# Kernel tuning notes

Measured on AMD Instinct MI355X. Metric: run time of the kernel, lower is better.

Reference implementation:

```python
import jax, jax.numpy as jnp
import numpy as np

M, K, N = 8192, 4096, 4096

def setup_inputs() -> dict:
    key = jax.random.key(0)
    k1, k2 = jax.random.split(key)
    x_q = jax.random.randint(k1, (M, K), -128, 128, dtype=jnp.int8)
    weight_q = jax.random.randint(k2, (N, K), -128, 128, dtype=jnp.int8)
    scale_x = jnp.float32(0.02)
    weight_scale = jnp.float32(1.0)
    out_scale = jnp.float32(1.0)
    return {"x_q": x_q, "scale_x": scale_x, "weight_q": weight_q,
            "weight_scale": weight_scale, "out_scale": out_scale}

def reference(x_q, scale_x, weight_q, weight_scale, out_scale):
    # int8 GEMM with int32 accumulation: [M,K] @ [K,N] -> [M,N] int32
    acc = jnp.matmul(x_q.astype(jnp.int32), weight_q.T.astype(jnp.int32))
    # fused dequant + requant scale, then round/clamp back to int8
    scale = scale_x * weight_scale / out_scale
    y = acc.astype(jnp.float32) * scale
    y_q = jnp.clip(jnp.round(y), -128, 127).astype(jnp.int8)
    return (y_q, out_scale)
```

## Files before the change

kernel.cpp:

```cpp
#include <hip/hip_runtime.h>
#include <stdint.h>

#define M_DIM 8192
#define K_DIM 4096
#define N_DIM 4096

typedef __attribute__((ext_vector_type(4))) int i32x4;

__global__ __launch_bounds__(256) void pack_kernel(const int* __restrict__ src,
                                                   int8_t* __restrict__ dst,
                                                   int n4) {
  const int stride = gridDim.x * 256;
  for (int i = blockIdx.x * 256 + threadIdx.x; i < n4; i += stride) {
    int4 v = reinterpret_cast<const int4*>(src)[i];
    int p = (v.x & 0xff) | ((v.y & 0xff) << 8) |
            ((v.z & 0xff) << 16) | ((v.w & 0xff) << 24);
    reinterpret_cast<int*>(dst)[i] = p;
  }
}

__global__ void tail_kernel(float* __restrict__ out, const float* __restrict__ so) {
  out[(size_t)M_DIM * N_DIM] = so[0];
}

#define BM2 256
#define BN2 256
#define BK2 128
#define NT  (K_DIM / BK2)

#define ASM_VMCNT0 asm volatile("s_waitcnt vmcnt(0)" ::: "memory")
#define ASM_LGKM0  asm volatile("s_waitcnt lgkmcnt(0)" ::: "memory")
#define BARRIER()  asm volatile("s_barrier" ::: "memory")
#define SCHEDB()   __builtin_amdgcn_sched_barrier(0)

#define STAGE(KT, BUF) do { \
  _Pragma("unroll") \
  for (int c_ = 0; c_ < 4; ++c_) { \
    const int8_t* ga_ = A8 + (size_t)(arow0 + c_*64 + srow) * K_DIM + (size_t)(KT)*BK2 + scol; \
    __builtin_amdgcn_global_load_lds((const __attribute__((address_space(1))) void*)ga_, \
        (__attribute__((address_space(3))) void*)(lds + (BUF)*65536 + c_*8192 + tid*16), 16, 0, 0); \
  } \
  _Pragma("unroll") \
  for (int c_ = 0; c_ < 4; ++c_) { \
    const int8_t* gb_ = B8 + (size_t)(bcol0 + c_*64 + srow) * K_DIM + (size_t)(KT)*BK2 + scol; \
    __builtin_amdgcn_global_load_lds((const __attribute__((address_space(1))) void*)gb_, \
        (__attribute__((address_space(3))) void*)(lds + (BUF)*65536 + 32768 + c_*8192 + tid*16), 16, 0, 0); \
  } } while (0)

__global__ __launch_bounds__(512, 2) void gemm2p(
    const int8_t* __restrict__ A8, const int8_t* __restrict__ B8,
    float* __restrict__ out,
    const float* __restrict__ sx, const float* __restrict__ sw,
    const float* __restrict__ so) {
  __shared__ __align__(16) int8_t lds[131072];

  const int tid = threadIdx.x;
  const int lane = tid & 63;
  const int wid = tid >> 6;
  const int wr = wid >> 2;
  const int wc = wid & 3;
  const int lrow = lane & 15;
  const int kq = lane >> 4;

  const int bid = blockIdx.x;
  const int wg = (bid & 7) * 64 + (bid >> 3);
  const int bm = wg & 31;
  const int bn = wg >> 5;
  const size_t arow0 = (size_t)bm * BM2;
  const size_t bcol0 = (size_t)bn * BN2;

  const int srow = tid >> 3;
  const int scol = (((tid & 7) ^ ((tid >> 3) & 7)) << 4);

  const int swz = (lrow & 7) << 4;
  const int pc0 = (0  + kq * 16) ^ swz;
  const int pc1 = (64 + kq * 16) ^ swz;
  const int aoff = (wr * 128 + lrow) * 128;
  const int boff = 32768 + (wc * 64 + lrow) * 128;

  i32x4 acc[8][4] = {};
  i32x4 af[8], bf[4];

  STAGE(0, 0);
  ASM_VMCNT0; BARRIER(); SCHEDB();

  for (int kt = 0; kt < NT; ++kt) {
    const int cb = kt & 1;
    const int8_t* abase = lds + cb * 65536 + aoff;
    const int8_t* bbase = lds + cb * 65536 + boff;
    if (kt < NT - 1) STAGE(kt + 1, cb ^ 1);

#pragma unroll
    for (int m = 0; m < 8; ++m) af[m] = *(const i32x4*)(abase + m * 2048 + pc0);
#pragma unroll
    for (int n = 0; n < 4; ++n) bf[n] = *(const i32x4*)(bbase + n * 2048 + pc0);
    ASM_LGKM0; SCHEDB();
    __builtin_amdgcn_s_setprio(1);
#pragma unroll
    for (int m = 0; m < 8; ++m)
#pragma unroll
      for (int n = 0; n < 4; ++n)
        acc[m][n] = __builtin_amdgcn_mfma_i32_16x16x64_i8(af[m], bf[n], acc[m][n], 0, 0, 0);
    __builtin_amdgcn_s_setprio(0);

#pragma unroll
    for (int m = 0; m < 8; ++m) af[m] = *(const i32x4*)(abase + m * 2048 + pc1);
#pragma unroll
    for (int n = 0; n < 4; ++n) bf[n] = *(const i32x4*)(bbase + n * 2048 + pc1);
    ASM_LGKM0; SCHEDB();
    __builtin_amdgcn_s_setprio(1);
#pragma unroll
    for (int m = 0; m < 8; ++m)
#pragma unroll
      for (int n = 0; n < 4; ++n)
        acc[m][n] = __builtin_amdgcn_mfma_i32_16x16x64_i8(af[m], bf[n], acc[m][n], 0, 0, 0);
    __builtin_amdgcn_s_setprio(0);

    ASM_VMCNT0; BARRIER(); SCHEDB();
  }

  const float s0 = *(volatile const float*)sx;
  const float s1 = *(volatile const float*)sw;
  const float s2 = *(volatile const float*)so;
  const float scale = s0 * s1 / s2;
#pragma unroll
  for (int m = 0; m < 8; ++m) {
#pragma unroll
    for (int n = 0; n < 4; ++n) {
#pragma unroll
      for (int j = 0; j < 4; ++j) {
        int gr = (int)arow0 + wr * 128 + m * 16 + kq * 4 + j;
        int gc = (int)bcol0 + wc * 64 + n * 16 + lrow;
        float v = rintf((float)acc[m][n][j] * scale);
        v = fminf(fmaxf(v, -128.f), 127.f);
        out[(size_t)gr * N_DIM + gc] = v;
      }
    }
  }
}

#define BM 128
#define BN 128
#define BK 64
__global__ __launch_bounds__(256) void gemm_direct(
    const int* __restrict__ A32, const int* __restrict__ B32,
    float* __restrict__ out,
    const float* __restrict__ sx, const float* __restrict__ sw,
    const float* __restrict__ so) {
  __shared__ int8_t As[BM * BK];
  __shared__ int8_t Bs[BN * BK];
  const int tid = threadIdx.x;
  const int lane = tid & 63;
  const int wid = tid >> 6;
  const int bid = blockIdx.x;
  const int bm = bid % (M_DIM / BM);
  const int bn = bid / (M_DIM / BM);
  const size_t arow0 = (size_t)bm * BM;
  const size_t bcol0 = (size_t)bn * BN;
  const int wrr = wid >> 1, wcc = wid & 1;
  const int lrow = lane & 15, kq = lane >> 4;
  i32x4 acc[4][4] = {};
  for (int kk = 0; kk < K_DIM; kk += BK) {
#pragma unroll
    for (int i = 0; i < 2; ++i) {
      int loff = i * 4096 + tid * 16;
      int r = loff >> 6, c = loff & 63;
      const int4* a4 = reinterpret_cast<const int4*>(A32 + (arow0 + r) * K_DIM + kk + c);
      const int4* b4 = reinterpret_cast<const int4*>(B32 + (bcol0 + r) * K_DIM + kk + c);
      int4 pa, pb;
      int4 t0 = a4[0], t1 = a4[1], t2 = a4[2], t3 = a4[3];
      pa.x = (t0.x & 0xff) | ((t0.y & 0xff) << 8) | ((t0.z & 0xff) << 16) | ((t0.w & 0xff) << 24);
      pa.y = (t1.x & 0xff) | ((t1.y & 0xff) << 8) | ((t1.z & 0xff) << 16) | ((t1.w & 0xff) << 24);
      pa.z = (t2.x & 0xff) | ((t2.y & 0xff) << 8) | ((t2.z & 0xff) << 16) | ((t2.w & 0xff) << 24);
      pa.w = (t3.x & 0xff) | ((t3.y & 0xff) << 8) | ((t3.z & 0xff) << 16) | ((t3.w & 0xff) << 24);
      t0 = b4[0]; t1 = b4[1]; t2 = b4[2]; t3 = b4[3];
      pb.x = (t0.x & 0xff) | ((t0.y & 0xff) << 8) | ((t0.z & 0xff) << 16) | ((t0.w & 0xff) << 24);
      pb.y = (t1.x & 0xff) | ((t1.y & 0xff) << 8) | ((t1.z & 0xff) << 16) | ((t1.w & 0xff) << 24);
      pb.z = (t2.x & 0xff) | ((t2.y & 0xff) << 8) | ((t2.z & 0xff) << 16) | ((t2.w & 0xff) << 24);
      pb.w = (t3.x & 0xff) | ((t3.y & 0xff) << 8) | ((t3.z & 0xff) << 16) | ((t3.w & 0xff) << 24);
      *reinterpret_cast<int4*>(As + loff) = pa;
      *reinterpret_cast<int4*>(Bs + loff) = pb;
    }
    __syncthreads();
    i32x4 afr[4], bfr[4];
#pragma unroll
    for (int m = 0; m < 4; ++m)
      afr[m] = *reinterpret_cast<const i32x4*>(As + (wrr * 64 + m * 16 + lrow) * BK + kq * 16);
#pragma unroll
    for (int n = 0; n < 4; ++n)
      bfr[n] = *reinterpret_cast<const i32x4*>(Bs + (wcc * 64 + n * 16 + lrow) * BK + kq * 16);
#pragma unroll
    for (int m = 0; m < 4; ++m)
#pragma unroll
      for (int n = 0; n < 4; ++n)
        acc[m][n] = __builtin_amdgcn_mfma_i32_16x16x64_i8(afr[m], bfr[n], acc[m][n], 0, 0, 0);
    __syncthreads();
  }
  const float scale = sx[0] * sw[0] / so[0];
#pragma unroll
  for (int m = 0; m < 4; ++m)
#pragma unroll
    for (int n = 0; n < 4; ++n)
#pragma unroll
      for (int j = 0; j < 4; ++j) {
        int gr = (int)arow0 + wrr * 64 + m * 16 + kq * 4 + j;
        int gc = (int)bcol0 + wcc * 64 + n * 16 + lrow;
        float v = rintf((float)acc[m][n][j] * scale);
        v = fminf(fmaxf(v, -128.f), 127.f);
        out[(size_t)gr * N_DIM + gc] = v;
      }
}

extern "C" void kernel_launch(void* const* d_in, const int* in_sizes, int n_in,
                              void* d_out, int out_size, void* d_ws, size_t ws_size,
                              hipStream_t stream) {
  const int* x32 = (const int*)d_in[0];
  const float* sx = (const float*)d_in[1];
  const int* w32 = (const int*)d_in[2];
  const float* sw = (const float*)d_in[3];
  const float* so = (const float*)d_in[4];
  float* out = (float*)d_out;

  tail_kernel<<<1, 1, 0, stream>>>(out, so);

  const size_t a_bytes = (size_t)M_DIM * K_DIM;
  const size_t b_bytes = (size_t)N_DIM * K_DIM;

  if (ws_size >= a_bytes + b_bytes) {
    int8_t* A8 = (int8_t*)d_ws;
    int8_t* B8 = A8 + a_bytes;
    pack_kernel<<<2048, 256, 0, stream>>>(x32, A8, (int)(a_bytes / 4));
    pack_kernel<<<2048, 256, 0, stream>>>(w32, B8, (int)(b_bytes / 4));
    const int grid = (M_DIM / BM2) * (N_DIM / BN2);
    gemm2p<<<grid, 512, 0, stream>>>(A8, B8, out, sx, sw, so);
  } else {
    const int grid = (M_DIM / BM) * (N_DIM / BN);
    gemm_direct<<<grid, 256, 0, stream>>>(x32, w32, out, sx, sw, so);
  }
}
```

Measured before the change: 401.2 us.

## Split tile loads into quadrants and interleave with sub-tile MFMA phases

Restructures the int8 GEMM main loop into four phases, each computing one quadrant of the 256x256 tile while the next k-tile's A/B halves are streamed into the other LDS buffer. Partial vmcnt waits replace the full drain, so global-to-LDS loads overlap compute at finer granularity. Each warp's fragment mapping changes to interleaved 64x32 sub-blocks, and both K halves are read together. The cost is more barriers per iteration and more registers for the doubled fragment arrays.

```diff
diff --git a/kernel.cpp b/kernel.cpp
--- a/kernel.cpp
+++ b/kernel.cpp
@@ -28,26 +28,58 @@
 #define BK2 128
 #define NT  (K_DIM / BK2)
 
-#define ASM_VMCNT0 asm volatile("s_waitcnt vmcnt(0)" ::: "memory")
-#define ASM_LGKM0  asm volatile("s_waitcnt lgkmcnt(0)" ::: "memory")
-#define BARRIER()  asm volatile("s_barrier" ::: "memory")
-#define SCHEDB()   __builtin_amdgcn_sched_barrier(0)
-
-#define STAGE(KT, BUF) do { \
-  _Pragma("unroll") \
-  for (int c_ = 0; c_ < 4; ++c_) { \
-    const int8_t* ga_ = A8 + (size_t)(arow0 + c_*64 + srow) * K_DIM + (size_t)(KT)*BK2 + scol; \
-    __builtin_amdgcn_global_load_lds((const __attribute__((address_space(1))) void*)ga_, \
-        (__attribute__((address_space(3))) void*)(lds + (BUF)*65536 + c_*8192 + tid*16), 16, 0, 0); \
-  } \
-  _Pragma("unroll") \
-  for (int c_ = 0; c_ < 4; ++c_) { \
-    const int8_t* gb_ = B8 + (size_t)(bcol0 + c_*64 + srow) * K_DIM + (size_t)(KT)*BK2 + scol; \
-    __builtin_amdgcn_global_load_lds((const __attribute__((address_space(1))) void*)gb_, \
-        (__attribute__((address_space(3))) void*)(lds + (BUF)*65536 + 32768 + c_*8192 + tid*16), 16, 0, 0); \
-  } } while (0)
-
-__global__ __launch_bounds__(512, 2) void gemm2p(
+#define ASM_VMCNT(N) asm volatile("s_waitcnt vmcnt(" #N ")" ::: "memory")
+#define ASM_LGKM0    asm volatile("s_waitcnt lgkmcnt(0)" ::: "memory")
+#define BARRIER()    asm volatile("s_barrier" ::: "memory")
+#define SCHEDB()     __builtin_amdgcn_sched_barrier(0)
+
+#define STAGE_A(KT, H, BUF) do { \
+  _Pragma("unroll") \
+  for (int c_ = 0; c_ < 2; ++c_) { \
+    const int8_t* g_ = A8 + (size_t)(arow0 + (H)*128 + c_*64 + srow) * K_DIM + (size_t)(KT)*BK2 + scol; \
+    __builtin_amdgcn_global_load_lds((const __attribute__((address_space(1))) void*)g_, \
+        (__attribute__((address_space(3))) void*)(lds + (BUF)*65536 + (H)*16384 + c_*8192 + tid*16), 16, 0, 0); \
+  } } while (0)
+
+#define STAGE_B(KT, H, BUF) do { \
+  _Pragma("unroll") \
+  for (int c_ = 0; c_ < 2; ++c_) { \
+    const int8_t* g_ = B8 + (size_t)(bcol0 + (H)*128 + c_*64 + srow) * K_DIM + (size_t)(KT)*BK2 + scol; \
+    __builtin_amdgcn_global_load_lds((const __attribute__((address_space(1))) void*)g_, \
+        (__attribute__((address_space(3))) void*)(lds + (BUF)*65536 + 32768 + (H)*16384 + c_*8192 + tid*16), 16, 0, 0); \
+  } } while (0)
+
+#define READ_AF(MH, AB) do { \
+  _Pragma("unroll") \
+  for (int m_ = 0; m_ < 4; ++m_) { \
+    const int8_t* p_ = (AB) + (MH)*16384 + m_*2048; \
+    af[(MH)*4 + m_][0] = *(const i32x4*)(p_ + pc0); \
+    af[(MH)*4 + m_][1] = *(const i32x4*)(p_ + pc1); \
+  } } while (0)
+
+#define READ_BF(NH, BB) do { \
+  _Pragma("unroll") \
+  for (int n_ = 0; n_ < 2; ++n_) { \
+    const int8_t* p_ = (BB) + (NH)*16384 + n_*2048; \
+    bf[(NH)*2 + n_][0] = *(const i32x4*)(p_ + pc0); \
+    bf[(NH)*2 + n_][1] = *(const i32x4*)(p_ + pc1); \
+  } } while (0)
+
+#define MMA16(MH, NH) do { \
+  __builtin_amdgcn_s_setprio(1); \
+  _Pragma("unroll") \
+  for (int m_ = 0; m_ < 4; ++m_) \
+    _Pragma("unroll") \
+    for (int n_ = 0; n_ < 2; ++n_) { \
+      acc[(MH)*4 + m_][(NH)*2 + n_] = __builtin_amdgcn_mfma_i32_16x16x64_i8( \
+          af[(MH)*4 + m_][0], bf[(NH)*2 + n_][0], acc[(MH)*4 + m_][(NH)*2 + n_], 0, 0, 0); \
+      acc[(MH)*4 + m_][(NH)*2 + n_] = __builtin_amdgcn_mfma_i32_16x16x64_i8( \
+          af[(MH)*4 + m_][1], bf[(NH)*2 + n_][1], acc[(MH)*4 + m_][(NH)*2 + n_], 0, 0, 0); \
+    } \
+  __builtin_amdgcn_s_setprio(0); \
+} while (0)
+
+__global__ __launch_bounds__(512, 2) void gemm8p(
     const int8_t* __restrict__ A8, const int8_t* __restrict__ B8,
     float* __restrict__ out,
     const float* __restrict__ sx, const float* __restrict__ sw,
@@ -75,48 +107,55 @@
   const int swz = (lrow & 7) << 4;
   const int pc0 = (0  + kq * 16) ^ swz;
   const int pc1 = (64 + kq * 16) ^ swz;
-  const int aoff = (wr * 128 + lrow) * 128;
-  const int boff = 32768 + (wc * 64 + lrow) * 128;
+  const int aoff = (wr * 64 + lrow) * 128;
+  const int boff = 32768 + (wc * 32 + lrow) * 128;
 
   i32x4 acc[8][4] = {};
-  i32x4 af[8], bf[4];
-
-  STAGE(0, 0);
-  ASM_VMCNT0; BARRIER(); SCHEDB();
-
-  for (int kt = 0; kt < NT; ++kt) {
+  i32x4 af[8][2], bf[4][2];
+
+  STAGE_A(0, 0, 0); STAGE_B(0, 0, 0); STAGE_B(0, 1, 0); STAGE_A(0, 1, 0);
+
+  for (int kt = 0; kt < NT - 1; ++kt) {
     const int cb = kt & 1;
-    const int8_t* abase = lds + cb * 65536 + aoff;
-    const int8_t* bbase = lds + cb * 65536 + boff;
-    if (kt < NT - 1) STAGE(kt + 1, cb ^ 1);
-
-#pragma unroll
-    for (int m = 0; m < 8; ++m) af[m] = *(const i32x4*)(abase + m * 2048 + pc0);
-#pragma unroll
-    for (int n = 0; n < 4; ++n) bf[n] = *(const i32x4*)(bbase + n * 2048 + pc0);
-    ASM_LGKM0; SCHEDB();
-    __builtin_amdgcn_s_setprio(1);
-#pragma unroll
-    for (int m = 0; m < 8; ++m)
-#pragma unroll
-      for (int n = 0; n < 4; ++n)
-        acc[m][n] = __builtin_amdgcn_mfma_i32_16x16x64_i8(af[m], bf[n], acc[m][n], 0, 0, 0);
-    __builtin_amdgcn_s_setprio(0);
-
-#pragma unroll
-    for (int m = 0; m < 8; ++m) af[m] = *(const i32x4*)(abase + m * 2048 + pc1);
-#pragma unroll
-    for (int n = 0; n < 4; ++n) bf[n] = *(const i32x4*)(bbase + n * 2048 + pc1);
-    ASM_LGKM0; SCHEDB();
-    __builtin_amdgcn_s_setprio(1);
-#pragma unroll
-    for (int m = 0; m < 8; ++m)
-#pragma unroll
-      for (int n = 0; n < 4; ++n)
-        acc[m][n] = __builtin_amdgcn_mfma_i32_16x16x64_i8(af[m], bf[n], acc[m][n], 0, 0, 0);
-    __builtin_amdgcn_s_setprio(0);
-
-    ASM_VMCNT0; BARRIER(); SCHEDB();
+    const int pb = cb ^ 1;
+    const int8_t* ab = lds + cb * 65536 + aoff;
+    const int8_t* bb = lds + cb * 65536 + boff;
+    ASM_VMCNT(4); BARRIER(); SCHEDB();
+    READ_AF(0, ab); READ_BF(0, bb);
+    STAGE_A(kt + 1, 0, pb);
+    ASM_LGKM0; SCHEDB();
+    MMA16(0, 0);
+    ASM_VMCNT(4); BARRIER(); SCHEDB();
+    READ_BF(1, bb);
+    STAGE_B(kt + 1, 0, pb);
+    ASM_LGKM0; SCHEDB();
+    MMA16(0, 1);
+    ASM_VMCNT(4); BARRIER(); SCHEDB();
+    READ_AF(1, ab);
+    STAGE_B(kt + 1, 1, pb);
+    ASM_LGKM0; SCHEDB();
+    MMA16(1, 0);
+    BARRIER(); SCHEDB();
+    STAGE_A(kt + 1, 1, pb);
+    MMA16(1, 1);
+  }
+  {
+    const int cb = (NT - 1) & 1;
+    const int8_t* ab = lds + cb * 65536 + aoff;
+    const int8_t* bb = lds + cb * 65536 + boff;
+    ASM_VMCNT(4); BARRIER(); SCHEDB();
+    READ_AF(0, ab); READ_BF(0, bb);
+    ASM_LGKM0; SCHEDB();
+    MMA16(0, 0);
+    ASM_VMCNT(2); BARRIER(); SCHEDB();
+    READ_BF(1, bb);
+    ASM_LGKM0; SCHEDB();
+    MMA16(0, 1);
+    ASM_VMCNT(0); BARRIER(); SCHEDB();
+    READ_AF(1, ab);
+    ASM_LGKM0; SCHEDB();
+    MMA16(1, 0);
+    MMA16(1, 1);
   }
 
   const float s0 = *(volatile const float*)sx;
@@ -124,14 +163,14 @@
   const float s2 = *(volatile const float*)so;
   const float scale = s0 * s1 / s2;
 #pragma unroll
-  for (int m = 0; m < 8; ++m) {
-#pragma unroll
-    for (int n = 0; n < 4; ++n) {
+  for (int am = 0; am < 8; ++am) {
+#pragma unroll
+    for (int bn2 = 0; bn2 < 4; ++bn2) {
 #pragma unroll
       for (int j = 0; j < 4; ++j) {
-        int gr = (int)arow0 + wr * 128 + m * 16 + kq * 4 + j;
-        int gc = (int)bcol0 + wc * 64 + n * 16 + lrow;
-        float v = rintf((float)acc[m][n][j] * scale);
+        int gr = (int)arow0 + (am >> 2) * 128 + wr * 64 + (am & 3) * 16 + kq * 4 + j;
+        int gc = (int)bcol0 + (bn2 >> 1) * 128 + wc * 32 + (bn2 & 1) * 16 + lrow;
+        float v = rintf((float)acc[am][bn2][j] * scale);
         v = fminf(fmaxf(v, -128.f), 127.f);
         out[(size_t)gr * N_DIM + gc] = v;
       }
@@ -232,7 +271,7 @@
     pack_kernel<<<2048, 256, 0, stream>>>(x32, A8, (int)(a_bytes / 4));
     pack_kernel<<<2048, 256, 0, stream>>>(w32, B8, (int)(b_bytes / 4));
     const int grid = (M_DIM / BM2) * (N_DIM / BN2);
-    gemm2p<<<grid, 512, 0, stream>>>(A8, B8, out, sx, sw, so);
+    gemm8p<<<grid, 512, 0, stream>>>(A8, B8, out, sx, sw, so);
   } else {
     const int grid = (M_DIM / BM) * (N_DIM / BN);
     gemm_direct<<<grid, 256, 0, stream>>>(x32, w32, out, sx, sw, so);
```

After: 399.9 us. No clear change (-0.3%).
